# Optimization experiments

Hardware: AMD Instinct MI355X
Metric: run time of the kernel (lower is better)

Reference implementation:

```python
import jax, jax.numpy as jnp
import numpy as np

N_CLUSTERS = 256  # must match fill_max of `clusters`
ALPHA = 7.18
MIN_MEMBERS = 4.0  # clusters with fewer members are dropped (as in original)


def setup_inputs() -> dict:
    key = jax.random.key(0)
    k1, k2 = jax.random.split(key)
    outputs = jax.random.normal(k1, (8192, 2048), dtype=jnp.float32)
    clusters = jax.random.randint(k2, (8192,), 0, N_CLUSTERS, dtype=jnp.int32)
    return {"outputs": outputs, "clusters": clusters}


def _magnet_loss(outputs, clusters):
    # outputs: [N, D] float32, clusters: [N] int32 in [0, N_CLUSTERS)
    n = outputs.shape[0]
    ones = jnp.ones((n,), jnp.float32)
    counts = jax.ops.segment_sum(ones, clusters, num_segments=N_CLUSTERS)          # [C]
    sums = jax.ops.segment_sum(outputs, clusters, num_segments=N_CLUSTERS)         # [C, D]
    means = sums / jnp.maximum(counts, 1.0)[:, None]                               # [C, D]
    valid = counts >= MIN_MEMBERS                                                   # [C] clusters kept
    inst_valid = valid[clusters]                                                    # [N]

    # residual norms to own-cluster mean (UNSQUARED L2, as in original)
    resid = outputs - means[clusters]                                               # [N, D]
    resid_norm = jnp.sqrt(jnp.sum(resid * resid, axis=1))                           # [N]

    num_instances = jnp.sum(jnp.where(valid, counts, 0.0))
    # original quirk: stdev = (sum of norms)^2 / num_instances
    stdev = jnp.square(jnp.sum(jnp.where(inst_valid, resid_norm, 0.0))) / num_instances

    # pairwise instance-to-mean L2 distances via GEMM: [N, C]
    sq = (jnp.sum(outputs * outputs, axis=1)[:, None]
          - 2.0 * (outputs @ means.T)
          + jnp.sum(means * means, axis=1)[None, :])
    dist = jnp.sqrt(jnp.maximum(sq, 0.0))                                           # [N, C]

    expd = jnp.exp(-0.5 * dist / stdev)                                             # [N, C]
    # denominator: sum over valid clusters other than own cluster
    other = jnp.arange(N_CLUSTERS, dtype=clusters.dtype)[None, :] != clusters[:, None]
    mask = valid[None, :] & other                                                   # [N, C]
    denom = jnp.sum(jnp.where(mask, expd, 0.0), axis=1)                             # [N]

    log_num = -0.5 * resid_norm / stdev - ALPHA                                     # [N]
    loss_i = jnp.log(denom) - log_num                                               # -log(exp(log_num)/denom)
    loss = jnp.sum(jnp.where(inst_valid, loss_i, 0.0)) / num_instances
    return loss.reshape(1)


def reference(outputs, clusters):
    return _magnet_loss(outputs.astype(jnp.float32), clusters)
```

## Files before the change

### kernel.cpp

```cpp
#include <hip/hip_runtime.h>
#include <hip/hip_bf16.h>
#include <math.h>

#define NROWS 8192
#define DIM   2048
#define NC    256
#define ALPHA_C 7.18f

typedef float  f32x4  __attribute__((ext_vector_type(4)));
typedef __bf16 bf16x8 __attribute__((ext_vector_type(8)));

#define OFF_A      (size_t)0
#define OFF_DOT    ((size_t)32 << 20)
#define OFF_B      ((size_t)40 << 20)
#define OFF_PERM   ((size_t)41 << 20)
#define OFF_MISC   (OFF_PERM + 32768)
#define OFF_GCTR   (OFF_MISC)
#define OFF_MN2    (OFF_MISC + 1024)
#define OFF_SCAL   (OFF_MISC + 2048)
#define OFF_CNT    (OFF_MISC + 3072)
#define OFF_BASE   (OFF_MISC + 4096)
#define OFF_ON2    (OFF_MISC + 5120)

__device__ __forceinline__ float wave_red_sum(float v) {
#pragma unroll
  for (int off = 32; off > 0; off >>= 1) v += __shfl_xor(v, off, 64);
  return v;
}

__global__ __launch_bounds__(256) void k_counts(const int* __restrict__ clu,
                                                float* __restrict__ counts,
                                                int* __restrict__ base,
                                                float* scal) {
  __shared__ int cnt[NC];
  __shared__ int pre[NC];
  __shared__ float part[4];
  int tid = threadIdx.x;
  cnt[tid] = 0;
  __syncthreads();
  for (int i = tid; i < NROWS; i += 256) atomicAdd(&cnt[clu[i]], 1);
  __syncthreads();
  int c = cnt[tid];
  counts[tid] = (float)c;
  pre[tid] = c;
  __syncthreads();
  for (int off = 1; off < NC; off <<= 1) {
    int v = (tid >= off) ? pre[tid - off] : 0;
    __syncthreads();
    pre[tid] += v;
    __syncthreads();
  }
  base[tid] = pre[tid] - c;
  float v = (c >= 4) ? (float)c : 0.0f;
  v = wave_red_sum(v);
  if ((tid & 63) == 0) part[tid >> 6] = v;
  __syncthreads();
  if (tid == 0) scal[1] = part[0] + part[1] + part[2] + part[3];
}

__global__ __launch_bounds__(256) void k_perm(const int* __restrict__ clu,
                                              const int* __restrict__ base,
                                              int* __restrict__ gctr,
                                              int* __restrict__ perm) {
  int i = blockIdx.x * 256 + threadIdx.x;
  int c = clu[i];
  int r = atomicAdd(&gctr[c], 1);
  perm[base[c] + r] = i;
}

__global__ __launch_bounds__(256) void k_msum(const float* __restrict__ out,
                                              const int* __restrict__ perm,
                                              const int* __restrict__ base,
                                              const float* __restrict__ counts,
                                              __bf16* __restrict__ B,
                                              float* __restrict__ mn2) {
  __shared__ int pr[64];
  __shared__ float part[4];
  int bid = blockIdx.x;
  int c = bid >> 3, sl = bid & 7;
  int tid = threadIdx.x;
  int col = sl * 256 + tid;
  int cnt = (int)counts[c];
  int b0 = base[c];
  float acc = 0.f;
  for (int r0 = 0; r0 < cnt; r0 += 64) {
    int lim = min(64, cnt - r0);
    if (tid < lim) pr[tid] = perm[b0 + r0 + tid];
    __syncthreads();
    for (int r = 0; r < lim; ++r) acc += out[(size_t)pr[r] * DIM + col];
    __syncthreads();
  }
  float mean = acc / fmaxf((float)cnt, 1.f);
  int nt = c >> 4, kk = col >> 5, lane = ((col >> 3) & 3) * 16 + (c & 15), j = col & 7;
  B[(((size_t)nt * 64 + kk) * 64 + lane) * 8 + j] = (__bf16)mean;
  float s = mean * mean;
  s = wave_red_sum(s);
  if ((tid & 63) == 0) part[tid >> 6] = s;
  __syncthreads();
  if (tid == 0) atomicAdd(&mn2[c], part[0] + part[1] + part[2] + part[3]);
}

__global__ __launch_bounds__(256) void k_conv(const float* __restrict__ out,
                                              bf16x8* __restrict__ A,
                                              float* __restrict__ onorm2) {
  __shared__ float part[4];
  int r = blockIdx.x, tid = threadIdx.x;
  const f32x4* src = (const f32x4*)(out + (size_t)r * DIM);
  f32x4 v0 = src[tid * 2], v1 = src[tid * 2 + 1];
  float s = 0.f;
  bf16x8 b;
#pragma unroll
  for (int j = 0; j < 4; ++j) { float f = v0[j]; s += f * f; b[j] = (__bf16)f; }
#pragma unroll
  for (int j = 0; j < 4; ++j) { float f = v1[j]; s += f * f; b[4 + j] = (__bf16)f; }
  int mt = r >> 4, kk = tid >> 2, lane = (tid & 3) * 16 + (r & 15);
  A[((size_t)mt * 64 + kk) * 64 + lane] = b;
  s = wave_red_sum(s);
  if ((tid & 63) == 0) part[tid >> 6] = s;
  __syncthreads();
  if (tid == 0) onorm2[r] = part[0] + part[1] + part[2] + part[3];
}

__global__ __launch_bounds__(256) void k_gemm(const bf16x8* __restrict__ A,
                                              const bf16x8* __restrict__ B,
                                              float* __restrict__ dot) {
  int bid = blockIdx.x;
  int wg = (bid & 7) * 32 + (bid >> 3);
  int bm = wg >> 2, bn = wg & 3;
  int w = threadIdx.x >> 6, l = threadIdx.x & 63;
  int mt0 = bm * 8 + w * 2;
  int nt0 = bn * 4;
  const bf16x8* Ap = A + (size_t)mt0 * 64 * 64 + l;
  const bf16x8* Bp = B + (size_t)nt0 * 64 * 64 + l;
  f32x4 acc[2][4] = {};
  for (int kk = 0; kk < 64; ++kk) {
    bf16x8 a0 = Ap[kk * 64];
    bf16x8 a1 = Ap[4096 + kk * 64];
    bf16x8 b0 = Bp[kk * 64];
    bf16x8 b1 = Bp[4096 + kk * 64];
    bf16x8 b2 = Bp[8192 + kk * 64];
    bf16x8 b3 = Bp[12288 + kk * 64];
    acc[0][0] = __builtin_amdgcn_mfma_f32_16x16x32_bf16(a0, b0, acc[0][0], 0, 0, 0);
    acc[0][1] = __builtin_amdgcn_mfma_f32_16x16x32_bf16(a0, b1, acc[0][1], 0, 0, 0);
    acc[0][2] = __builtin_amdgcn_mfma_f32_16x16x32_bf16(a0, b2, acc[0][2], 0, 0, 0);
    acc[0][3] = __builtin_amdgcn_mfma_f32_16x16x32_bf16(a0, b3, acc[0][3], 0, 0, 0);
    acc[1][0] = __builtin_amdgcn_mfma_f32_16x16x32_bf16(a1, b0, acc[1][0], 0, 0, 0);
    acc[1][1] = __builtin_amdgcn_mfma_f32_16x16x32_bf16(a1, b1, acc[1][1], 0, 0, 0);
    acc[1][2] = __builtin_amdgcn_mfma_f32_16x16x32_bf16(a1, b2, acc[1][2], 0, 0, 0);
    acc[1][3] = __builtin_amdgcn_mfma_f32_16x16x32_bf16(a1, b3, acc[1][3], 0, 0, 0);
  }
  int r0 = bm * 128 + w * 32 + (l >> 4) * 4;
  int cb = bn * 64 + (l & 15);
#pragma unroll
  for (int m = 0; m < 2; ++m)
#pragma unroll
    for (int reg = 0; reg < 4; ++reg) {
      float* dst = dot + (size_t)(r0 + m * 16 + reg) * NC + cb;
#pragma unroll
      for (int n = 0; n < 4; ++n) dst[n * 16] = acc[m][n][reg];
    }
}

__global__ __launch_bounds__(256) void k_resid2(const float* __restrict__ dot,
                                                const int* __restrict__ clu,
                                                const float* __restrict__ onorm2,
                                                const float* __restrict__ mnorm2,
                                                const float* __restrict__ counts,
                                                float* scal) {
  __shared__ float part[4];
  int tid = threadIdx.x;
  int i = blockIdx.x * 256 + tid;
  int ci = clu[i];
  float dv = dot[(size_t)i * NC + ci];
  float rn = sqrtf(fmaxf(onorm2[i] - 2.f * dv + mnorm2[ci], 0.f));
  float v = (counts[ci] >= 4.0f) ? rn : 0.f;
  v = wave_red_sum(v);
  if ((tid & 63) == 0) part[tid >> 6] = v;
  __syncthreads();
  if (tid == 0) atomicAdd(&scal[0], part[0] + part[1] + part[2] + part[3]);
}

__global__ void k_stdev(float* scal) {
  scal[2] = scal[0] * scal[0] / scal[1];
}

__global__ __launch_bounds__(256) void k_denom(const float* __restrict__ dot,
                                               const int* __restrict__ clu,
                                               const float* __restrict__ on2v,
                                               const float* __restrict__ mn2,
                                               const float* __restrict__ counts,
                                               float* scal) {
  __shared__ float part[4];
  int w = threadIdx.x >> 6, l = threadIdx.x & 63;
  float cfac = -0.5f / scal[2];
  f32x4 mn = ((const f32x4*)mn2)[l];
  f32x4 cn = ((const f32x4*)counts)[l];
  float lsum = 0.f;
  int i0 = blockIdx.x * 32 + w * 8;
  for (int t = 0; t < 8; ++t) {
    int i = i0 + t;
    int ci = clu[i];
    float on2 = on2v[i];
    f32x4 dv = ((const f32x4*)(dot + (size_t)i * NC))[l];
    float dsum = 0.f;
#pragma unroll
    for (int j = 0; j < 4; ++j) {
      int cc = l * 4 + j;
      float dist = sqrtf(fmaxf(on2 - 2.f * dv[j] + mn[j], 0.f));
      float e = __expf(cfac * dist);
      dsum += ((cn[j] >= 4.0f) && (cc != ci)) ? e : 0.f;
    }
    dsum = wave_red_sum(dsum);
    if (l == 0 && counts[ci] >= 4.0f) {
      float dvi = dot[(size_t)i * NC + ci];
      float rn = sqrtf(fmaxf(on2 - 2.f * dvi + mn2[ci], 0.f));
      lsum += __logf(dsum) - (cfac * rn - ALPHA_C);
    }
  }
  lsum = wave_red_sum(lsum);
  if (l == 0) part[w] = lsum;
  __syncthreads();
  if (threadIdx.x == 0) atomicAdd(&scal[3], part[0] + part[1] + part[2] + part[3]);
}

__global__ void k_final(const float* scal, float* out) {
  out[0] = scal[3] / scal[1];
}

extern "C" void kernel_launch(void* const* d_in, const int* in_sizes, int n_in,
                              void* d_out, int out_size, void* d_ws, size_t ws_size,
                              hipStream_t stream) {
  const float* outputs = (const float*)d_in[0];
  const int* clusters = (const int*)d_in[1];
  float* out = (float*)d_out;
  char* ws = (char*)d_ws;

  bf16x8* A      = (bf16x8*)(ws + OFF_A);
  float*  dotb   = (float*)(ws + OFF_DOT);
  __bf16* B      = (__bf16*)(ws + OFF_B);
  int*    perm   = (int*)(ws + OFF_PERM);
  int*    gctr   = (int*)(ws + OFF_GCTR);
  float*  mn2    = (float*)(ws + OFF_MN2);
  float*  scal   = (float*)(ws + OFF_SCAL);
  float*  counts = (float*)(ws + OFF_CNT);
  int*    base   = (int*)(ws + OFF_BASE);
  float*  on2    = (float*)(ws + OFF_ON2);

  hipMemsetAsync(ws + OFF_GCTR, 0, 3072, stream);
  k_counts<<<1, 256, 0, stream>>>(clusters, counts, base, scal);
  k_perm<<<NROWS / 256, 256, 0, stream>>>(clusters, base, gctr, perm);
  k_conv<<<NROWS, 256, 0, stream>>>(outputs, A, on2);
  k_msum<<<NC * 8, 256, 0, stream>>>(outputs, perm, base, counts, B, mn2);
  k_gemm<<<256, 256, 0, stream>>>(A, (const bf16x8*)B, dotb);
  k_resid2<<<NROWS / 256, 256, 0, stream>>>(dotb, clusters, on2, mn2, counts, scal);
  k_stdev<<<1, 1, 0, stream>>>(scal);
  k_denom<<<NROWS / 32, 256, 0, stream>>>(dotb, clusters, on2, mn2, counts, scal);
  k_final<<<1, 1, 0, stream>>>(scal, out);
}
```

Before: 198.0 us.

## Parallelize cluster histogram and restructure bf16 conversion to write contiguous tiles

Replaces the single-block cluster counting kernel with a multi-block histogram (shared atomics, then global atomics into a zeroed buffer) followed by a small scan kernel. Rewrites the fp32-to-bf16 conversion so that each block handles a 16-row tile and writes its packed A tile contiguously, with row norms reduced through shared memory. This cuts the serial work in the count step and makes the A stores coalesced. The cost is an extra kernel launch and less regular row reads in the conversion kernel.

Measured after the change: 179.4 us. 1.1x faster.

```diff
diff --git a/kernel.cpp b/kernel.cpp
--- a/kernel.cpp
+++ b/kernel.cpp
@@ -18,9 +18,10 @@
 #define OFF_GCTR   (OFF_MISC)
 #define OFF_MN2    (OFF_MISC + 1024)
 #define OFF_SCAL   (OFF_MISC + 2048)
-#define OFF_CNT    (OFF_MISC + 3072)
-#define OFF_BASE   (OFF_MISC + 4096)
-#define OFF_ON2    (OFF_MISC + 5120)
+#define OFF_HIST   (OFF_MISC + 3072)
+#define OFF_CNT    (OFF_MISC + 4096)
+#define OFF_BASE   (OFF_MISC + 5120)
+#define OFF_ON2    (OFF_MISC + 6144)
 
 __device__ __forceinline__ float wave_red_sum(float v) {
 #pragma unroll
@@ -28,19 +29,25 @@
   return v;
 }
 
-__global__ __launch_bounds__(256) void k_counts(const int* __restrict__ clu,
-                                                float* __restrict__ counts,
-                                                int* __restrict__ base,
-                                                float* scal) {
-  __shared__ int cnt[NC];
+__global__ __launch_bounds__(256) void k_hist(const int* __restrict__ clu,
+                                              int* __restrict__ hist) {
+  __shared__ int h[NC];
+  int tid = threadIdx.x;
+  h[tid] = 0;
+  __syncthreads();
+  atomicAdd(&h[clu[blockIdx.x * 256 + tid]], 1);
+  __syncthreads();
+  if (h[tid]) atomicAdd(&hist[tid], h[tid]);
+}
+
+__global__ __launch_bounds__(256) void k_scan(const int* __restrict__ hist,
+                                              float* __restrict__ counts,
+                                              int* __restrict__ base,
+                                              float* scal) {
   __shared__ int pre[NC];
   __shared__ float part[4];
   int tid = threadIdx.x;
-  cnt[tid] = 0;
-  __syncthreads();
-  for (int i = tid; i < NROWS; i += 256) atomicAdd(&cnt[clu[i]], 1);
-  __syncthreads();
-  int c = cnt[tid];
+  int c = hist[tid];
   counts[tid] = (float)c;
   pre[tid] = c;
   __syncthreads();
@@ -103,22 +110,34 @@
 __global__ __launch_bounds__(256) void k_conv(const float* __restrict__ out,
                                               bf16x8* __restrict__ A,
                                               float* __restrict__ onorm2) {
-  __shared__ float part[4];
-  int r = blockIdx.x, tid = threadIdx.x;
-  const f32x4* src = (const f32x4*)(out + (size_t)r * DIM);
-  f32x4 v0 = src[tid * 2], v1 = src[tid * 2 + 1];
-  float s = 0.f;
-  bf16x8 b;
-#pragma unroll
-  for (int j = 0; j < 4; ++j) { float f = v0[j]; s += f * f; b[j] = (__bf16)f; }
-#pragma unroll
-  for (int j = 0; j < 4; ++j) { float f = v1[j]; s += f * f; b[4 + j] = (__bf16)f; }
-  int mt = r >> 4, kk = tid >> 2, lane = (tid & 3) * 16 + (r & 15);
-  A[((size_t)mt * 64 + kk) * 64 + lane] = b;
-  s = wave_red_sum(s);
-  if ((tid & 63) == 0) part[tid >> 6] = s;
-  __syncthreads();
-  if (tid == 0) onorm2[r] = part[0] + part[1] + part[2] + part[3];
+  __shared__ float lsum[256];
+  int mt = blockIdx.x, tid = threadIdx.x;
+  int r = tid & 15;
+  const float* rowp = out + ((size_t)mt * 16 + r) * DIM;
+  bf16x8* At = A + (size_t)mt * 4096;
+  float acc = 0.f;
+#pragma unroll 4
+  for (int s = 0; s < 16; ++s) {
+    int q = s * 256 + tid;
+    int kk = q >> 6, lane = q & 63;
+    int d = kk * 32 + (lane >> 4) * 8;
+    const f32x4* src = (const f32x4*)(rowp + d);
+    f32x4 v0 = src[0], v1 = src[1];
+    bf16x8 b;
+#pragma unroll
+    for (int j = 0; j < 4; ++j) { float f = v0[j]; acc += f * f; b[j] = (__bf16)f; }
+#pragma unroll
+    for (int j = 0; j < 4; ++j) { float f = v1[j]; acc += f * f; b[4 + j] = (__bf16)f; }
+    At[q] = b;
+  }
+  lsum[tid] = acc;
+  __syncthreads();
+  if (tid < 16) {
+    float s = 0.f;
+#pragma unroll
+    for (int k = 0; k < 16; ++k) s += lsum[tid + 16 * k];
+    onorm2[mt * 16 + tid] = s;
+  }
 }
 
 __global__ __launch_bounds__(256) void k_gemm(const bf16x8* __restrict__ A,
@@ -242,14 +261,16 @@
   int*    gctr   = (int*)(ws + OFF_GCTR);
   float*  mn2    = (float*)(ws + OFF_MN2);
   float*  scal   = (float*)(ws + OFF_SCAL);
+  int*    hist   = (int*)(ws + OFF_HIST);
   float*  counts = (float*)(ws + OFF_CNT);
   int*    base   = (int*)(ws + OFF_BASE);
   float*  on2    = (float*)(ws + OFF_ON2);
 
-  hipMemsetAsync(ws + OFF_GCTR, 0, 3072, stream);
-  k_counts<<<1, 256, 0, stream>>>(clusters, counts, base, scal);
+  hipMemsetAsync(ws + OFF_GCTR, 0, 4096, stream);
+  k_hist<<<NROWS / 256, 256, 0, stream>>>(clusters, hist);
+  k_scan<<<1, 256, 0, stream>>>(hist, counts, base, scal);
   k_perm<<<NROWS / 256, 256, 0, stream>>>(clusters, base, gctr, perm);
-  k_conv<<<NROWS, 256, 0, stream>>>(outputs, A, on2);
+  k_conv<<<NROWS / 16, 256, 0, stream>>>(outputs, A, on2);
   k_msum<<<NC * 8, 256, 0, stream>>>(outputs, perm, base, counts, B, mn2);
   k_gemm<<<256, 256, 0, stream>>>(A, (const bf16x8*)B, dotb);
   k_resid2<<<NROWS / 256, 256, 0, stream>>>(dotb, clusters, on2, mn2, counts, scal);
```
